# Kernel optimization log

Measured on AMD Instinct MI355X. Metric: run time of the kernel, lower is better.

## Reference

```python
import jax, jax.numpy as jnp
import numpy as np

MAX_BLUR = 20.0
MIN_BLUR = 0.5
MIN_SCALE = 0.001


def _dct_matrix(N, dtype):
    """Orthonormal DCT-II matrix C: dct(v) = C @ v (matches torch_dct norm='ortho')."""
    n = jnp.arange(N, dtype=dtype)
    k = n[:, None]
    C = jnp.cos(jnp.pi * (n[None, :] + 0.5) * k / N)
    scale = jnp.where(k == 0, jnp.sqrt(jnp.asarray(1.0 / N, dtype)), jnp.sqrt(jnp.asarray(2.0 / N, dtype)))
    return C * scale


def setup_inputs() -> dict:
    key = jax.random.key(0)
    k1, k2 = jax.random.split(key)
    x = jax.random.normal(k1, (128, 3, 256, 256), dtype=jnp.float32)
    t = jax.random.uniform(k2, (128,), dtype=jnp.float32)
    return {"x": x, "t": t}


def reference(x, t):
    dtype = x.dtype
    N = x.shape[-1]
    # frequency grid: pi * linspace(0, N-1, N) / N, squared and summed over 2D
    freqs = jnp.pi * jnp.arange(N, dtype=dtype) / N
    freq_sq = freqs[:, None] ** 2 + freqs[None, :] ** 2  # [N, N]

    # blur schedule: exp(log(min_blur)*(1-t) + log(max_blur)*t)
    sigmas = jnp.exp(np.log(MIN_BLUR) * (1.0 - t) + np.log(MAX_BLUR) * t)
    sigmas = sigmas[:, None, None, None]  # [B,1,1,1]
    tau = sigmas ** 2 / 2

    fade_freq = jnp.exp(-freq_sq * tau)  # [B,1,N,N]
    fade_freq = jnp.where(fade_freq < 0.01, jnp.zeros((), dtype), fade_freq)

    C = _dct_matrix(N, dtype)  # [N, N]
    # separable 2D DCT-II (ortho): out[k,n] = sum_{h,w} C[k,h] C[n,w] x[h,w]
    dct_x = jnp.einsum('kh,nw,bchw->bckn', C, C, x)
    blurred_dct = dct_x * (fade_freq * (1.0 - MIN_SCALE) + MIN_SCALE)
    # inverse 2D DCT (ortho): transpose matrices
    blurred_x = jnp.einsum('kh,nw,bckn->bchw', C, C, blurred_dct)
    return blurred_x.astype(dtype)
```

## Files before the change

### kernel.cpp

```cpp
#include <hip/hip_runtime.h>
#include <hip/hip_fp16.h>

typedef _Float16 f16;
typedef _Float16 f16x4 __attribute__((ext_vector_type(4)));
typedef _Float16 f16x8 __attribute__((ext_vector_type(8)));
typedef float f32x16 __attribute__((ext_vector_type(16)));

#define NSZ 256
#define NIMG 384

__device__ __forceinline__ int sw(int r, int c) { return r * NSZ + (c ^ ((r & 15) << 3)); }

__device__ __forceinline__ int frag_off(int r, int c) {
  return (((((r >> 5) * 16 + (c >> 4)) << 6) + (((c >> 3) & 1) << 5) + (r & 31)) << 3) + (c & 7);
}

__device__ __forceinline__ unsigned pk2(float a, float b) {
  unsigned r;
  asm("v_cvt_pkrtz_f16_f32 %0, %1, %2" : "=v"(r) : "v"(a), "v"(b));
  return r;
}
__device__ __forceinline__ void swap32(unsigned& a, unsigned& b) {
  asm("v_permlane32_swap_b32 %0, %1" : "+v"(a), "+v"(b));
}

#define TBL_FRAG(Tf, tile, q, lane) (*(const f16x8*)&(Tf)[((((tile) * 16 + (q)) << 6) + (lane)) << 3])
#define MFMA32(a, b, c) __builtin_amdgcn_mfma_f32_32x32x16_f16((a), (b), (c), 0, 0, 0)

__device__ __forceinline__ void frag_store(f16* __restrict__ dst, int tile, int chunk0,
                                           const f32x16& a, int lane) {
  unsigned d[8];
#pragma unroll
  for (int v2 = 0; v2 < 4; ++v2) {
    d[v2 * 2 + 0] = pk2(a[v2 * 4 + 0], a[v2 * 4 + 1]);
    d[v2 * 2 + 1] = pk2(a[v2 * 4 + 2], a[v2 * 4 + 3]);
  }
#pragma unroll
  for (int vp = 0; vp < 2; ++vp) {
    unsigned A0 = d[vp * 4 + 0], B0 = d[vp * 4 + 2];
    unsigned A1 = d[vp * 4 + 1], B1 = d[vp * 4 + 3];
    swap32(A0, B0);
    swap32(A1, B1);
    uint4 st = {A0, A1, B0, B1};
    *(uint4*)&dst[(((tile * 16 + (chunk0 + vp)) << 6) + lane) << 3] = st;
  }
}

__global__ void prep_kernel(f16* __restrict__ Cf, f16* __restrict__ CTf,
                            float* __restrict__ g, int* __restrict__ Kq,
                            const float* __restrict__ t) {
  int k = blockIdx.x;
  int h = threadIdx.x;
  double scale = (k == 0) ? 0.0625 : 0.08838834764831844;
  double val = cos(3.14159265358979323846 * ((double)h + 0.5) * (double)k / 256.0) * scale;
  f16 vh = (f16)((float)val);
  Cf[frag_off(k, h)] = vh;
  CTf[frag_off(h, k)] = vh;
  int pred = 0;
  if (k < 128) {
    float tb = t[k];
    float sg = expf(-0.69314718055994531f * (1.0f - tb) + 2.99573227355399099f * tb);
    float tau = 0.5f * sg * sg;
    float f = 3.14159265358979f * (float)h / 256.0f;
    float gv = expf(-f * f * tau);
    g[k * NSZ + h] = gv;
    pred = (gv >= 0.0099f) ? 1 : 0;
  }
  int cnt = __syncthreads_count(pred);
  if (k < 128 && h == 0) {
    int K = ((cnt + 31) >> 5) << 5;
    if (K < 32) K = 32;
    if (K > 256) K = 256;
    Kq[k] = K;
  }
}

__global__ __launch_bounds__(256, 4) void kernelS1(
    const float* __restrict__ x, f16* __restrict__ Vf, const f16* __restrict__ Cf,
    const int* __restrict__ KqA) {
  __shared__ f16 Xs[64 * NSZ];

  int bid = blockIdx.x;
  int wg = (bid & 7) * 192 + (bid >> 3);
  int img = wg >> 2, hb = wg & 3;
  int b = img / 3;
  int Kq = KqA[b];
  int t = threadIdx.x, lane = t & 63, wave = t >> 6;
  int l31 = lane & 31, hi = lane >> 5, kh = hi * 8;
  const float* X = x + (size_t)img * 65536 + hb * 64 * NSZ;
  f16* Vo = Vf + (size_t)img * 65536;

#pragma unroll
  for (int bt = 0; bt < 2; ++bt) {
    float4 xv[8];
#pragma unroll
    for (int i = 0; i < 8; ++i)
      xv[i] = *(const float4*)&X[bt * 8192 + i * 1024 + t * 4];
#pragma unroll
    for (int i = 0; i < 8; ++i) {
      int flat = bt * 8192 + i * 1024 + t * 4;
      int r = flat >> 8, c = flat & 255;
      union { unsigned u[2]; f16x4 h; } v;
      v.u[0] = pk2(xv[i].x, xv[i].y);
      v.u[1] = pk2(xv[i].z, xv[i].w);
      *(f16x4*)&Xs[sw(r, c)] = v.h;
    }
  }
  __syncthreads();

  int n0 = wave * 64;
  if (n0 >= Kq) return;
  const f32x16 zz = {0.f, 0.f, 0.f, 0.f, 0.f, 0.f, 0.f, 0.f,
                     0.f, 0.f, 0.f, 0.f, 0.f, 0.f, 0.f, 0.f};
  f32x16 acc[2][2];
#pragma unroll
  for (int fi = 0; fi < 2; ++fi)
#pragma unroll
    for (int fj = 0; fj < 2; ++fj) acc[fi][fj] = zz;

  bool act1 = (n0 + 32) < Kq;
#pragma unroll 4
  for (int q = 0; q < 16; ++q) {
    f16x8 a[2];
#pragma unroll
    for (int fi = 0; fi < 2; ++fi)
      a[fi] = *(const f16x8*)&Xs[sw(fi * 32 + l31, q * 16 + kh)];
    {
      f16x8 bf = TBL_FRAG(Cf, wave * 2 + 0, q, lane);
      acc[0][0] = MFMA32(a[0], bf, acc[0][0]);
      acc[1][0] = MFMA32(a[1], bf, acc[1][0]);
    }
    if (act1) {
      f16x8 bf = TBL_FRAG(Cf, wave * 2 + 1, q, lane);
      acc[0][1] = MFMA32(a[0], bf, acc[0][1]);
      acc[1][1] = MFMA32(a[1], bf, acc[1][1]);
    }
  }
#pragma unroll
  for (int fj = 0; fj < 2; ++fj) {
    if (n0 + fj * 32 >= Kq) continue;
#pragma unroll
    for (int fi = 0; fi < 2; ++fi)
      frag_store(Vo, wave * 2 + fj, hb * 4 + fi * 2, acc[fi][fj], lane);
  }
}

__global__ __launch_bounds__(256, 4) void kernelS2(
    const f16* __restrict__ Vf, f16* __restrict__ Ef,
    const f16* __restrict__ Cf, const float* __restrict__ g,
    const int* __restrict__ KqA) {
  int bid = blockIdx.x;
  int wg = (bid & 7) * 192 + (bid >> 3);
  int img = wg >> 2, nb = wg & 3;
  int b = img / 3;
  int Kq = KqA[b];
  if (nb * 64 >= Kq) return;
  int t = threadIdx.x, lane = t & 63, wave = t >> 6;
  int l31 = lane & 31, hi = lane >> 5, hi4 = hi * 4;
  int nt = wave & 1, kq = wave >> 1;
  int n0 = nb * 64 + nt * 32;
  if (n0 >= Kq) return;
  const f16* Vi = Vf + (size_t)img * 65536;
  f16* Eo = Ef + (size_t)img * 65536;

  const f32x16 zz = {0.f, 0.f, 0.f, 0.f, 0.f, 0.f, 0.f, 0.f,
                     0.f, 0.f, 0.f, 0.f, 0.f, 0.f, 0.f, 0.f};
  f32x16 acc[4];
#pragma unroll
  for (int fj = 0; fj < 4; ++fj) acc[fj] = zz;

  int ktiles = Kq >> 5;
#pragma unroll 4
  for (int q = 0; q < 16; ++q) {
    f16x8 a = TBL_FRAG(Vi, nb * 2 + nt, q, lane);
#pragma unroll
    for (int fj = 0; fj < 4; ++fj) {
      int kt = kq * 4 + fj;
      if (kt < ktiles) {
        f16x8 bf = TBL_FRAG(Cf, kt, q, lane);
        acc[fj] = MFMA32(a, bf, acc[fj]);
      }
    }
  }

  const float* gb = g + b * NSZ;
  float gn[16];
#pragma unroll
  for (int v2 = 0; v2 < 4; ++v2) {
    float4 g4 = *(const float4*)&gb[n0 + v2 * 8 + hi4];
    gn[v2 * 4 + 0] = g4.x; gn[v2 * 4 + 1] = g4.y;
    gn[v2 * 4 + 2] = g4.z; gn[v2 * 4 + 3] = g4.w;
  }
#pragma unroll
  for (int fj = 0; fj < 4; ++fj) {
    int kt = kq * 4 + fj;
    if (kt >= ktiles) continue;
    float gk = gb[kt * 32 + l31];
    f32x16 sv;
#pragma unroll
    for (int e16 = 0; e16 < 16; ++e16) {
      float fade = gk * gn[e16];
      float s = ((fade < 0.01f) ? 0.f : fade) * 0.999f + 0.001f;
      sv[e16] = acc[fj][e16] * s;
    }
    frag_store(Eo, kt, (nb * 2 + nt) * 2, sv, lane);
  }
}

__global__ __launch_bounds__(256, 5) void kernelS3(
    const f16* __restrict__ Ef, float* __restrict__ out, const f16* __restrict__ CTf,
    const int* __restrict__ KqA) {
  __shared__ f16 G[64 * NSZ];

  int bid = blockIdx.x;
  int wg = (bid & 7) * 192 + (bid >> 3);
  int img = wg >> 2, wb = wg & 3;
  int b = img / 3;
  int Kq = KqA[b], nq = Kq >> 4;
  int t = threadIdx.x, lane = t & 63, wave = t >> 6;
  int l31 = lane & 31, hi = lane >> 5, kh = hi * 8, hi4 = hi * 4;
  const f16* Ei = Ef + (size_t)img * 65536;
  float* Y = out + (size_t)img * 65536;

  const f32x16 zz = {0.f, 0.f, 0.f, 0.f, 0.f, 0.f, 0.f, 0.f,
                     0.f, 0.f, 0.f, 0.f, 0.f, 0.f, 0.f, 0.f};
  f32x16 acc[2][2];
#pragma unroll
  for (int fi = 0; fi < 2; ++fi)
#pragma unroll
    for (int fj = 0; fj < 2; ++fj) acc[fi][fj] = zz;

  bool act0 = (wave * 2 + 0) * 32 < Kq;
  bool act1 = (wave * 2 + 1) * 32 < Kq;
  if (act0) {
#pragma unroll 4
    for (int q = 0; q < nq; ++q) {
      f16x8 a0 = TBL_FRAG(Ei, wave * 2 + 0, q, lane);
      f16x8 a1;
      if (act1) a1 = TBL_FRAG(Ei, wave * 2 + 1, q, lane);
#pragma unroll
      for (int fj = 0; fj < 2; ++fj) {
        f16x8 bf = TBL_FRAG(CTf, wb * 2 + fj, q, lane);
        acc[0][fj] = MFMA32(a0, bf, acc[0][fj]);
        if (act1) acc[1][fj] = MFMA32(a1, bf, acc[1][fj]);
      }
    }
#pragma unroll
    for (int fi = 0; fi < 2; ++fi) {
      if ((wave * 2 + fi) * 32 >= Kq) continue;
      int colbase = (wave * 2 + fi) * 32;
#pragma unroll
      for (int fj = 0; fj < 2; ++fj) {
        int crow = fj * 32 + l31;
#pragma unroll
        for (int v2 = 0; v2 < 4; ++v2) {
          f16x4 hv;
          hv[0] = (f16)acc[fi][fj][v2 * 4 + 0];
          hv[1] = (f16)acc[fi][fj][v2 * 4 + 1];
          hv[2] = (f16)acc[fi][fj][v2 * 4 + 2];
          hv[3] = (f16)acc[fi][fj][v2 * 4 + 3];
          *(f16x4*)&G[sw(crow, colbase + v2 * 8 + hi4)] = hv;
        }
      }
    }
  }
  __syncthreads();

#pragma unroll
  for (int fi = 0; fi < 2; ++fi)
#pragma unroll
    for (int fj = 0; fj < 2; ++fj) acc[fi][fj] = zz;
#pragma unroll 4
  for (int q = 0; q < nq; ++q) {
    f16x8 a0 = TBL_FRAG(CTf, wave * 2 + 0, q, lane);
    f16x8 a1 = TBL_FRAG(CTf, wave * 2 + 1, q, lane);
#pragma unroll
    for (int fj = 0; fj < 2; ++fj) {
      f16x8 bf = *(const f16x8*)&G[sw(fj * 32 + l31, q * 16 + kh)];
      acc[0][fj] = MFMA32(a0, bf, acc[0][fj]);
      acc[1][fj] = MFMA32(a1, bf, acc[1][fj]);
    }
  }
#pragma unroll
  for (int fi = 0; fi < 2; ++fi)
#pragma unroll
    for (int fj = 0; fj < 2; ++fj) {
      int w = wb * 64 + fj * 32 + l31;
#pragma unroll
      for (int v2 = 0; v2 < 4; ++v2)
#pragma unroll
        for (int e = 0; e < 4; ++e) {
          int h = (wave * 2 + fi) * 32 + v2 * 8 + hi4 + e;
          __builtin_nontemporal_store(acc[fi][fj][v2 * 4 + e], &Y[h * NSZ + w]);
        }
    }
}

extern "C" void kernel_launch(void* const* d_in, const int* in_sizes, int n_in,
                              void* d_out, int out_size, void* d_ws, size_t ws_size,
                              hipStream_t stream) {
  const float* x = (const float*)d_in[0];
  const float* t = (const float*)d_in[1];
  float* out = (float*)d_out;

  char* ws = (char*)d_ws;
  float* g = (float*)ws;
  f16* Cf = (f16*)(ws + 131072);
  f16* CTf = (f16*)(ws + 262144);
  int* Kq = (int*)(ws + 393216);
  f16* Ef = (f16*)(ws + 393728);
  f16* Vf = (f16*)d_out;

  prep_kernel<<<256, 256, 0, stream>>>(Cf, CTf, g, Kq, t);
  kernelS1<<<NIMG * 4, 256, 0, stream>>>(x, Vf, Cf, Kq);
  kernelS2<<<NIMG * 4, 256, 0, stream>>>(Vf, Ef, Cf, g, Kq);
  kernelS3<<<NIMG * 4, 256, 0, stream>>>(Ef, out, CTf, Kq);
}
```

Baseline: 104.1 us.

## Fuse first two DCT stages into one kernel with LDS-resident intermediate

Merges the row-DCT kernel and the column-DCT-plus-fade kernel into one kernel. Each block computes a 64-column slice of the first-stage product across all 256 rows, staging it in LDS instead of writing it to global memory and reading it back. This removes one kernel launch and the global round trip of the intermediate. In exchange, every block now reloads the whole input image (four n-blocks per image read the same x), the extra LDS buffer lowers occupancy (launch bounds drop to 2), and the 4-chunk loop adds serializing barriers.

```diff
diff --git a/kernel.cpp b/kernel.cpp
--- a/kernel.cpp
+++ b/kernel.cpp
@@ -75,110 +75,87 @@
   }
 }
 
-__global__ __launch_bounds__(256, 4) void kernelS1(
-    const float* __restrict__ x, f16* __restrict__ Vf, const f16* __restrict__ Cf,
+__global__ __launch_bounds__(256, 2) void kernelK1(
+    const float* __restrict__ x, f16* __restrict__ Ef,
+    const f16* __restrict__ Cf, const float* __restrict__ g,
     const int* __restrict__ KqA) {
   __shared__ f16 Xs[64 * NSZ];
-
-  int bid = blockIdx.x;
-  int wg = (bid & 7) * 192 + (bid >> 3);
-  int img = wg >> 2, hb = wg & 3;
-  int b = img / 3;
-  int Kq = KqA[b];
-  int t = threadIdx.x, lane = t & 63, wave = t >> 6;
-  int l31 = lane & 31, hi = lane >> 5, kh = hi * 8;
-  const float* X = x + (size_t)img * 65536 + hb * 64 * NSZ;
-  f16* Vo = Vf + (size_t)img * 65536;
-
-#pragma unroll
-  for (int bt = 0; bt < 2; ++bt) {
-    float4 xv[8];
-#pragma unroll
-    for (int i = 0; i < 8; ++i)
-      xv[i] = *(const float4*)&X[bt * 8192 + i * 1024 + t * 4];
-#pragma unroll
-    for (int i = 0; i < 8; ++i) {
-      int flat = bt * 8192 + i * 1024 + t * 4;
-      int r = flat >> 8, c = flat & 255;
-      union { unsigned u[2]; f16x4 h; } v;
-      v.u[0] = pk2(xv[i].x, xv[i].y);
-      v.u[1] = pk2(xv[i].z, xv[i].w);
-      *(f16x4*)&Xs[sw(r, c)] = v.h;
-    }
-  }
-  __syncthreads();
-
-  int n0 = wave * 64;
-  if (n0 >= Kq) return;
-  const f32x16 zz = {0.f, 0.f, 0.f, 0.f, 0.f, 0.f, 0.f, 0.f,
-                     0.f, 0.f, 0.f, 0.f, 0.f, 0.f, 0.f, 0.f};
-  f32x16 acc[2][2];
-#pragma unroll
-  for (int fi = 0; fi < 2; ++fi)
-#pragma unroll
-    for (int fj = 0; fj < 2; ++fj) acc[fi][fj] = zz;
-
-  bool act1 = (n0 + 32) < Kq;
-#pragma unroll 4
-  for (int q = 0; q < 16; ++q) {
-    f16x8 a[2];
-#pragma unroll
-    for (int fi = 0; fi < 2; ++fi)
-      a[fi] = *(const f16x8*)&Xs[sw(fi * 32 + l31, q * 16 + kh)];
-    {
-      f16x8 bf = TBL_FRAG(Cf, wave * 2 + 0, q, lane);
-      acc[0][0] = MFMA32(a[0], bf, acc[0][0]);
-      acc[1][0] = MFMA32(a[1], bf, acc[1][0]);
-    }
-    if (act1) {
-      f16x8 bf = TBL_FRAG(Cf, wave * 2 + 1, q, lane);
-      acc[0][1] = MFMA32(a[0], bf, acc[0][1]);
-      acc[1][1] = MFMA32(a[1], bf, acc[1][1]);
-    }
-  }
-#pragma unroll
-  for (int fj = 0; fj < 2; ++fj) {
-    if (n0 + fj * 32 >= Kq) continue;
-#pragma unroll
-    for (int fi = 0; fi < 2; ++fi)
-      frag_store(Vo, wave * 2 + fj, hb * 4 + fi * 2, acc[fi][fj], lane);
-  }
-}
-
-__global__ __launch_bounds__(256, 4) void kernelS2(
-    const f16* __restrict__ Vf, f16* __restrict__ Ef,
-    const f16* __restrict__ Cf, const float* __restrict__ g,
-    const int* __restrict__ KqA) {
+  __shared__ f16 Vl[64 * NSZ];
+
   int bid = blockIdx.x;
   int wg = (bid & 7) * 192 + (bid >> 3);
   int img = wg >> 2, nb = wg & 3;
   int b = img / 3;
   int Kq = KqA[b];
   if (nb * 64 >= Kq) return;
+
   int t = threadIdx.x, lane = t & 63, wave = t >> 6;
-  int l31 = lane & 31, hi = lane >> 5, hi4 = hi * 4;
-  int nt = wave & 1, kq = wave >> 1;
+  int l31 = lane & 31, hi = lane >> 5, kh = hi * 8, hi4 = hi * 4;
+  const float* X = x + (size_t)img * 65536;
+  f16* Eo = Ef + (size_t)img * 65536;
+
+  const f32x16 zz = {0.f, 0.f, 0.f, 0.f, 0.f, 0.f, 0.f, 0.f,
+                     0.f, 0.f, 0.f, 0.f, 0.f, 0.f, 0.f, 0.f};
+
+  int wh = wave >> 1, wn = wave & 1;
+  bool actn = (nb * 64 + wn * 32) < Kq;
+  for (int hc = 0; hc < 4; ++hc) {
+#pragma unroll
+    for (int bt = 0; bt < 2; ++bt) {
+      float4 xv[8];
+#pragma unroll
+      for (int i = 0; i < 8; ++i)
+        xv[i] = *(const float4*)&X[hc * 16384 + bt * 8192 + i * 1024 + t * 4];
+#pragma unroll
+      for (int i = 0; i < 8; ++i) {
+        int flat = bt * 8192 + i * 1024 + t * 4;
+        int r = flat >> 8, c = flat & 255;
+        union { unsigned u[2]; f16x4 h; } v;
+        v.u[0] = pk2(xv[i].x, xv[i].y);
+        v.u[1] = pk2(xv[i].z, xv[i].w);
+        *(f16x4*)&Xs[sw(r, c)] = v.h;
+      }
+    }
+    __syncthreads();
+    if (actn) {
+      f32x16 acc = zz;
+#pragma unroll 4
+      for (int q = 0; q < 16; ++q) {
+        f16x8 a = *(const f16x8*)&Xs[sw(wh * 32 + l31, q * 16 + kh)];
+        f16x8 bf = TBL_FRAG(Cf, nb * 2 + wn, q, lane);
+        acc = MFMA32(a, bf, acc);
+      }
+#pragma unroll
+      for (int v2 = 0; v2 < 4; ++v2) {
+        f16x4 hv;
+        hv[0] = (f16)acc[v2 * 4 + 0];
+        hv[1] = (f16)acc[v2 * 4 + 1];
+        hv[2] = (f16)acc[v2 * 4 + 2];
+        hv[3] = (f16)acc[v2 * 4 + 3];
+        *(f16x4*)&Vl[sw(wn * 32 + l31, hc * 64 + wh * 32 + v2 * 8 + hi4)] = hv;
+      }
+    }
+    __syncthreads();
+  }
+
+  int nt = wave & 1, kp = wave >> 1;
   int n0 = nb * 64 + nt * 32;
   if (n0 >= Kq) return;
-  const f16* Vi = Vf + (size_t)img * 65536;
-  f16* Eo = Ef + (size_t)img * 65536;
-
-  const f32x16 zz = {0.f, 0.f, 0.f, 0.f, 0.f, 0.f, 0.f, 0.f,
-                     0.f, 0.f, 0.f, 0.f, 0.f, 0.f, 0.f, 0.f};
-  f32x16 acc[4];
-#pragma unroll
-  for (int fj = 0; fj < 4; ++fj) acc[fj] = zz;
-
   int ktiles = Kq >> 5;
+
+  f32x16 acc2[4];
+#pragma unroll
+  for (int fj = 0; fj < 4; ++fj) acc2[fj] = zz;
+
 #pragma unroll 4
   for (int q = 0; q < 16; ++q) {
-    f16x8 a = TBL_FRAG(Vi, nb * 2 + nt, q, lane);
+    f16x8 a = *(const f16x8*)&Vl[sw(nt * 32 + l31, q * 16 + kh)];
 #pragma unroll
     for (int fj = 0; fj < 4; ++fj) {
-      int kt = kq * 4 + fj;
+      int kt = kp * 4 + fj;
       if (kt < ktiles) {
         f16x8 bf = TBL_FRAG(Cf, kt, q, lane);
-        acc[fj] = MFMA32(a, bf, acc[fj]);
+        acc2[fj] = MFMA32(a, bf, acc2[fj]);
       }
     }
   }
@@ -193,7 +170,7 @@
   }
 #pragma unroll
   for (int fj = 0; fj < 4; ++fj) {
-    int kt = kq * 4 + fj;
+    int kt = kp * 4 + fj;
     if (kt >= ktiles) continue;
     float gk = gb[kt * 32 + l31];
     f32x16 sv;
@@ -201,7 +178,7 @@
     for (int e16 = 0; e16 < 16; ++e16) {
       float fade = gk * gn[e16];
       float s = ((fade < 0.01f) ? 0.f : fade) * 0.999f + 0.001f;
-      sv[e16] = acc[fj][e16] * s;
+      sv[e16] = acc2[fj][e16] * s;
     }
     frag_store(Eo, kt, (nb * 2 + nt) * 2, sv, lane);
   }
@@ -309,10 +286,8 @@
   f16* CTf = (f16*)(ws + 262144);
   int* Kq = (int*)(ws + 393216);
   f16* Ef = (f16*)(ws + 393728);
-  f16* Vf = (f16*)d_out;
 
   prep_kernel<<<256, 256, 0, stream>>>(Cf, CTf, g, Kq, t);
-  kernelS1<<<NIMG * 4, 256, 0, stream>>>(x, Vf, Cf, Kq);
-  kernelS2<<<NIMG * 4, 256, 0, stream>>>(Vf, Ef, Cf, g, Kq);
+  kernelK1<<<NIMG * 4, 256, 0, stream>>>(x, Ef, Cf, g, Kq);
   kernelS3<<<NIMG * 4, 256, 0, stream>>>(Ef, out, CTf, Kq);
 }
```

Measured after the change: 105.5 us. Within noise of the previous version (+1.3%).
